# Performance work log

Hardware: AMD Instinct MI355X
Metric: run time of the kernel (lower is better)

Reference implementation:

```python
import jax, jax.numpy as jnp
import numpy as np

D_MODEL = 1024
NUM_HEADS = 16
D_K = D_MODEL // NUM_HEADS
ROPE_THETA = 10000.0


def apply_rope(x, positions):
    # x: (b, h, s, d_k), positions: (b, s) int
    half = D_K // 2
    inv_freq = ROPE_THETA ** (-jnp.arange(half, dtype=jnp.float32) * 2.0 / D_K)  # (half,)
    angles = positions[:, None, :, None].astype(jnp.float32) * inv_freq  # (b,1,s,half)
    cos, sin = jnp.cos(angles), jnp.sin(angles)
    x_even = x[..., 0::2]
    x_odd = x[..., 1::2]
    r_even = x_even * cos - x_odd * sin
    r_odd = x_even * sin + x_odd * cos
    # re-interleave
    out = jnp.stack([r_even, r_odd], axis=-1).reshape(x.shape)
    return out


def setup_inputs() -> dict:
    key = jax.random.key(0)
    k1, k2, k3, k4, k5 = jax.random.split(key, 5)
    b, s = 2, 2048
    scale = 1.0 / np.sqrt(D_MODEL)
    x = jax.random.normal(k1, (b, s, D_MODEL), dtype=jnp.float32)
    w_q = jax.random.normal(k2, (D_MODEL, D_MODEL), dtype=jnp.float32) * scale
    w_k = jax.random.normal(k3, (D_MODEL, D_MODEL), dtype=jnp.float32) * scale
    w_v = jax.random.normal(k4, (D_MODEL, D_MODEL), dtype=jnp.float32) * scale
    w_o = jax.random.normal(k5, (D_MODEL, D_MODEL), dtype=jnp.float32) * scale
    token_positions = jnp.broadcast_to(jnp.arange(s, dtype=jnp.int64 if jax.config.jax_enable_x64 else jnp.int32), (b, s))
    return {"x": x, "w_q": w_q, "w_k": w_k, "w_v": w_v, "w_o": w_o,
            "token_positions": token_positions}


def reference(x, w_q, w_k, w_v, w_o, token_positions):
    b, s, _ = x.shape
    # QKV projections: w_* are (h*d_k, d_model); y = x @ w^T
    def proj(w):
        y = jnp.einsum('bsd,ed->bse', x, w)  # (b,s,h*d_k)
        return y.reshape(b, s, NUM_HEADS, D_K).transpose(0, 2, 1, 3)  # (b,h,s,d_k)
    Q, K, V = proj(w_q), proj(w_k), proj(w_v)
    Q = apply_rope(Q, token_positions)
    K = apply_rope(K, token_positions)
    scores = jnp.einsum('bhqd,bhkd->bhqk', Q, K) / jnp.sqrt(jnp.float32(D_K))
    causal = jnp.tril(jnp.ones((s, s), dtype=bool))
    scores = jnp.where(causal[None, None], scores, -jnp.inf)
    attn = jax.nn.softmax(scores, axis=-1)
    out = jnp.einsum('bhqk,bhkd->bhqd', attn, V)  # (b,h,s,d_v)
    out = out.transpose(0, 2, 1, 3).reshape(b, s, NUM_HEADS * D_K)
    return jnp.einsum('bse,de->bsd', out, w_o)
```

## Files before the change

### kernel.cpp

```cpp
#include <hip/hip_runtime.h>

#define B_ 2
#define S_ 2048
#define DM 1024
#define NH 16
#define DK 64

using bf16x8  = __attribute__((ext_vector_type(8)))  short;
using f32x4   = __attribute__((ext_vector_type(4)))  float;

__device__ __forceinline__ float bf2f(short v){
  unsigned u = ((unsigned)(unsigned short)v) << 16;
  union { unsigned u; float f; } c; c.u = u; return c.f;
}
__device__ __forceinline__ short f2bf(float f){
  union { float f; unsigned u; } c; c.f = f;
  unsigned u = c.u + 0x7FFFu + ((c.u >> 16) & 1u);
  return (short)(u >> 16);
}
__device__ __forceinline__ unsigned packbf(float lo, float hi){
  union { float f; unsigned u; } a, b; a.f = lo; b.f = hi;
  return __builtin_amdgcn_perm(b.u, a.u, 0x07060302u);
}
__device__ __forceinline__ void gload16(const void* g, void* l){
  __builtin_amdgcn_global_load_lds(
    (const __attribute__((address_space(1))) unsigned*)g,
    (__attribute__((address_space(3))) unsigned*)l, 16, 0, 0);
}

__global__ void cast_rope(const float* __restrict__ x, const float* __restrict__ wq,
                          const float* __restrict__ wk, const float* __restrict__ wv,
                          const float* __restrict__ wo, const int* __restrict__ pos,
                          short* __restrict__ xb, short* __restrict__ wqkv,
                          short* __restrict__ wob, float* __restrict__ tab){
  const int bid = blockIdx.x;
  if (bid < 8192){
    int i = bid * 256 + threadIdx.x;
    const float4* src; short4* dst;
    if (i < (1 << 20)){
      src = (const float4*)x + i; dst = (short4*)xb + i;
    } else {
      int j = i - (1 << 20);
      int seg = j >> 18, off = j & ((1 << 18) - 1);
      const float* sp = seg == 0 ? wq : seg == 1 ? wk : seg == 2 ? wv : wo;
      short* dp = seg < 3 ? wqkv + ((size_t)seg << 20) : wob;
      src = (const float4*)sp + off; dst = (short4*)dp + off;
    }
    float4 v = *src;
    short4 o; o.x = f2bf(v.x); o.y = f2bf(v.y); o.z = f2bf(v.z); o.w = f2bf(v.w);
    *dst = o;
  } else {
    int idx = (bid - 8192) * 256 + threadIdx.x;
    int j = idx & 31, bs = idx >> 5;
    float p = (float)pos[bs];
    float inv = powf(10000.0f, -(float)(2 * j) / 64.0f);
    float ang = p * inv;
    tab[(size_t)bs * 64 + j]      = cosf(ang);
    tab[(size_t)bs * 64 + 32 + j] = sinf(ang);
  }
}

__launch_bounds__(512)
__global__ void gemm_qkv(const short* __restrict__ A, const short* __restrict__ Bm,
                         const float* __restrict__ tab,
                         short* __restrict__ Qr, short* __restrict__ Kr,
                         short* __restrict__ Vt){
  __shared__ short lds[3 * 8192];
  constexpr int K = 1024, NT = 32;
  const int tid = threadIdx.x;
  const int l = tid & 63, w = tid >> 6;
  const int lr = l & 15, lg = l >> 4;
  const int wr = w >> 2, wc = w & 3;
  const int wg  = blockIdx.y * gridDim.x + blockIdx.x;
  const int xcd = wg & 7, idx = wg >> 3;
  const int bn  = (xcd & 1) * 12 + idx % 12;
  const int bm  = (xcd >> 1) * 8 + idx / 12;
  const short* Ab = A  + (size_t)bm * 128 * K;
  const short* Bb = Bm + (size_t)bn * 128 * K;
  const int r0 = tid >> 2, c4 = tid & 3;
  f32x4 acc[4][2];
  #pragma unroll
  for (int m = 0; m < 4; ++m)
    #pragma unroll
    for (int n = 0; n < 2; ++n) acc[m][n] = (f32x4){0.f, 0.f, 0.f, 0.f};

  auto stage = [&](int t){
    short* buf = lds + (t % 3) * 8192;
    gload16(Ab + (size_t)r0 * K + t * 32 + c4 * 8, buf + tid * 8);
    gload16(Bb + (size_t)r0 * K + t * 32 + c4 * 8, buf + 4096 + tid * 8);
  };

  stage(0); stage(1);
  for (int t = 0; t < NT; ++t){
    if (t < NT - 1) asm volatile("s_waitcnt vmcnt(2)" ::: "memory");
    else            asm volatile("s_waitcnt vmcnt(0)" ::: "memory");
    __builtin_amdgcn_s_barrier();
    __builtin_amdgcn_sched_barrier(0);
    if (t + 2 < NT) stage(t + 2);
    const short* bufA = lds + (t % 3) * 8192;
    const short* bufB = bufA + 4096;
    bf16x8 a[4], bfr[2];
    #pragma unroll
    for (int m = 0; m < 4; ++m)
      a[m] = *(const bf16x8*)(bufA + (wr * 64 + m * 16 + lr) * 32 + lg * 8);
    #pragma unroll
    for (int n = 0; n < 2; ++n)
      bfr[n] = *(const bf16x8*)(bufB + (wc * 32 + n * 16 + lr) * 32 + lg * 8);
    __builtin_amdgcn_s_setprio(1);
    #pragma unroll
    for (int m = 0; m < 4; ++m)
      #pragma unroll
      for (int n = 0; n < 2; ++n)
        acc[m][n] = __builtin_amdgcn_mfma_f32_16x16x32_bf16(a[m], bfr[n], acc[m][n], 0, 0, 0);
    __builtin_amdgcn_s_setprio(0);
  }

  if (bn >= 16){
    __syncthreads();
    short* T = lds;
    #pragma unroll
    for (int m = 0; m < 4; ++m)
      #pragma unroll
      for (int n = 0; n < 2; ++n){
        const int col_l = wc * 32 + n * 16 + lr;
        const int row0  = wr * 64 + m * 16 + lg * 4;
        short4 pk;
        pk.x = f2bf(acc[m][n][0]); pk.y = f2bf(acc[m][n][1]);
        pk.z = f2bf(acc[m][n][2]); pk.w = f2bf(acc[m][n][3]);
        *(short4*)(T + col_l * 136 + row0) = pk;
      }
    __syncthreads();
    const int h0   = (bn - 16) * 2;
    const int tok0 = bm * 128;
    const int b    = tok0 >> 11, s0 = tok0 & 2047;
    const int col_l = tid >> 2;
    const int d  = col_l & 63;
    const int hh = h0 + (col_l >> 6);
    short* dstrow = Vt + ((size_t)(b * NH + hh) * DK + d) * S_ + s0;
    #pragma unroll
    for (int k = 0; k < 4; ++k){
      const int chunk = (tid & 3) * 4 + k;
      bf16x8 v = *(const bf16x8*)(T + col_l * 136 + chunk * 8);
      *(bf16x8*)(dstrow + chunk * 8) = v;
    }
  } else {
    #pragma unroll
    for (int m = 0; m < 4; ++m)
      #pragma unroll
      for (int n = 0; n < 2; ++n){
        const int col = bn * 128 + wc * 32 + n * 16 + lr;
        const int which = col >> 10;
        #pragma unroll
        for (int j = 0; j < 4; ++j){
          const int row = bm * 128 + wr * 64 + m * 16 + lg * 4 + j;
          float v = acc[m][n][j];
          const int d  = col & 63;
          const int dp = d >> 1;
          const float c = tab[(size_t)row * 64 + dp];
          const float s = tab[(size_t)row * 64 + 32 + dp];
          const float p = __shfl_xor(v, 1);
          float r = v * c + p * ((d & 1) ? s : -s);
          if (which == 0) r *= 0.125f;
          short* dst = which ? Kr : Qr;
          const int b = row >> 11, si = row & 2047;
          const int h = (col >> 6) & 15;
          dst[(((size_t)(b * NH + h)) * S_ + si) * DK + d] = f2bf(r);
        }
      }
  }
}

__launch_bounds__(512)
__global__ void gemm_o(const short* __restrict__ A, const short* __restrict__ Bm,
                       float* __restrict__ C){
  __shared__ short As[128 * 32];
  __shared__ short Bs[64 * 32];
  constexpr int K = 1024, N = 1024;
  const int tid = threadIdx.x;
  const int l = tid & 63, w = tid >> 6;
  const int lr = l & 15, lg = l >> 4;
  const int wr = w >> 2, wc = w & 3;
  const int nwg = gridDim.x * gridDim.y;
  const int wg  = blockIdx.y * gridDim.x + blockIdx.x;
  const int sw  = (wg & 7) * (nwg >> 3) + (wg >> 3);
  const int bn  = sw % gridDim.x, bm = sw / gridDim.x;
  const short* Ab = A  + (size_t)bm * 128 * K;
  const short* Bb = Bm + (size_t)bn * 64 * K;
  f32x4 acc[4];
  #pragma unroll
  for (int m = 0; m < 4; ++m) acc[m] = (f32x4){0.f, 0.f, 0.f, 0.f};
  const int r0 = tid >> 2, c4 = tid & 3;
  for (int kt = 0; kt < K; kt += 32){
    gload16(Ab + (size_t)r0 * K + kt + c4 * 8, As + tid * 8);
    if (tid < 256)
      gload16(Bb + (size_t)r0 * K + kt + c4 * 8, Bs + tid * 8);
    __syncthreads();
    bf16x8 a[4], bfr;
    #pragma unroll
    for (int m = 0; m < 4; ++m)
      a[m] = *(const bf16x8*)(As + (wr * 64 + m * 16 + lr) * 32 + lg * 8);
    bfr = *(const bf16x8*)(Bs + (wc * 16 + lr) * 32 + lg * 8);
    #pragma unroll
    for (int m = 0; m < 4; ++m)
      acc[m] = __builtin_amdgcn_mfma_f32_16x16x32_bf16(a[m], bfr, acc[m], 0, 0, 0);
    __syncthreads();
  }
  #pragma unroll
  for (int m = 0; m < 4; ++m)
    #pragma unroll
    for (int j = 0; j < 4; ++j){
      int row = bm * 128 + wr * 64 + m * 16 + lg * 4 + j;
      int col = bn * 64 + wc * 16 + lr;
      C[(size_t)row * N + col] = acc[m][j];
    }
}

__device__ __forceinline__ void attn_tile_step(
    const bf16x8 qa0, const bf16x8 qa1,
    f32x4 (&acc)[4], float& mrow, float& lsum,
    const short* Ks, const short* Vs, unsigned* pw,
    int diagmask, int lr, int lg, int wl){
  float sv[4][4];
  __builtin_amdgcn_s_setprio(1);
  #pragma unroll
  for (int n = 0; n < 4; ++n){
    const int R = n * 16 + lr;
    const int c0 = lg ^ (R & 7);
    bf16x8 k0 = *(const bf16x8*)(Ks + R * 64 + c0 * 8);
    bf16x8 k1 = *(const bf16x8*)(Ks + R * 64 + (c0 ^ 4) * 8);
    f32x4 z = (f32x4){0.f, 0.f, 0.f, 0.f};
    z = __builtin_amdgcn_mfma_f32_16x16x32_bf16(k0, qa0, z, 0, 0, 0);
    z = __builtin_amdgcn_mfma_f32_16x16x32_bf16(k1, qa1, z, 0, 0, 0);
    #pragma unroll
    for (int j = 0; j < 4; ++j) sv[n][j] = z[j];
  }
  __builtin_amdgcn_s_setprio(0);
  if (diagmask){
    const int qloc = wl * 16 + lr;
    #pragma unroll
    for (int n = 0; n < 4; ++n)
      #pragma unroll
      for (int j = 0; j < 4; ++j)
        if (n * 16 + lg * 4 + j > qloc) sv[n][j] = -1e30f;
  }
  float lm = sv[0][0];
  #pragma unroll
  for (int n = 0; n < 4; ++n)
    #pragma unroll
    for (int j = 0; j < 4; ++j) lm = fmaxf(lm, sv[n][j]);
  lm = fmaxf(lm, __shfl_xor(lm, 16));
  lm = fmaxf(lm, __shfl_xor(lm, 32));
  if (!__all(lm <= mrow + 8.f)){
    float mnew = fmaxf(mrow, lm);
    float corr = __expf(mrow - mnew);
    mrow = mnew;
    lsum *= corr;
    float cb[4];
    #pragma unroll
    for (int j = 0; j < 4; ++j) cb[j] = __shfl(corr, lg * 4 + j);
    #pragma unroll
    for (int n = 0; n < 4; ++n)
      #pragma unroll
      for (int j = 0; j < 4; ++j) acc[n][j] *= cb[j];
  }
  float psum = 0.f;
  #pragma unroll
  for (int n = 0; n < 4; ++n)
    #pragma unroll
    for (int j = 0; j < 4; ++j){
      float p = __expf(sv[n][j] - mrow);
      sv[n][j] = p; psum += p;
    }
  psum += __shfl_xor(psum, 16);
  psum += __shfl_xor(psum, 32);
  lsum += psum;
  const int swz = (lr & 7) << 2;
  #pragma unroll
  for (int n = 0; n < 4; ++n){
    pw[lr * 32 + ((n * 8 + lg * 2 + 0) ^ swz)] = packbf(sv[n][0], sv[n][1]);
    pw[lr * 32 + ((n * 8 + lg * 2 + 1) ^ swz)] = packbf(sv[n][2], sv[n][3]);
  }
  bf16x8 pa0 = *(const bf16x8*)(pw + lr * 32 + ((lg * 4) ^ swz));
  bf16x8 pa1 = *(const bf16x8*)(pw + lr * 32 + ((16 + lg * 4) ^ swz));
  __builtin_amdgcn_s_setprio(1);
  #pragma unroll
  for (int n = 0; n < 4; ++n){
    const int R = n * 16 + lr;
    const int c0 = lg ^ (R & 7);
    bf16x8 v0 = *(const bf16x8*)(Vs + R * 64 + c0 * 8);
    bf16x8 v1 = *(const bf16x8*)(Vs + R * 64 + (c0 ^ 4) * 8);
    acc[n] = __builtin_amdgcn_mfma_f32_16x16x32_bf16(pa0, v0, acc[n], 0, 0, 0);
    acc[n] = __builtin_amdgcn_mfma_f32_16x16x32_bf16(pa1, v1, acc[n], 0, 0, 0);
  }
  __builtin_amdgcn_s_setprio(0);
}

__launch_bounds__(512)
__global__ void attn_kernel(const short* __restrict__ Qr, const short* __restrict__ Kr,
                            const short* __restrict__ Vt, short* __restrict__ AO){
  __shared__ short Ks[2][64 * 64];
  __shared__ short Vs[2][64 * 64];
  __shared__ unsigned Pw[8][16 * 32];
  const int tid = threadIdx.x;
  const int l = tid & 63, w = tid >> 6;
  const int lr = l & 15, lg = l >> 4;
  const int wl = w & 3, wgp = w >> 2;
  const int bid = blockIdx.x;
  const int qp = bid >> 5;
  const int bh = (((bid >> 3) & 3) << 3) | (bid & 7);
  const int h = bh & 15, b = bh >> 4;
  const int t0 = qp, t1 = 31 - qp;
  const int myqt = wgp ? t0 : t1;
  const short* Qp = Qr + (size_t)bh * S_ * DK;
  const short* Kp = Kr + (size_t)bh * S_ * DK;
  const short* Vp = Vt + (size_t)bh * DK * S_;

  bf16x8 qa0, qa1;
  {
    const short* q0 = Qp + (size_t)(myqt * 64 + wl * 16 + lr) * DK + lg * 8;
    qa0 = *(const bf16x8*)q0; qa1 = *(const bf16x8*)(q0 + 32);
  }
  f32x4 acc[4];
  float ms = -1e30f, ls = 0.f;
  #pragma unroll
  for (int n = 0; n < 4; ++n) acc[n] = (f32x4){0.f, 0.f, 0.f, 0.f};
  unsigned* pw = &Pw[w][0];
  const int r0 = tid >> 3, q8 = tid & 7;
  const int sq8 = q8 ^ (r0 & 7);

  gload16(Kp + (size_t)r0 * DK + sq8 * 8, &Ks[0][tid * 8]);
  gload16(Vp + (size_t)r0 * S_ + sq8 * 8, &Vs[0][tid * 8]);
  int cur = 0;
  for (int kt = 0; kt <= t1; ++kt){
    __syncthreads();
    if (kt < t1){
      gload16(Kp + (size_t)((kt + 1) * 64 + r0) * DK + sq8 * 8, &Ks[cur ^ 1][tid * 8]);
      gload16(Vp + (size_t)r0 * S_ + (kt + 1) * 64 + sq8 * 8,   &Vs[cur ^ 1][tid * 8]);
    }
    if (kt <= myqt)
      attn_tile_step(qa0, qa1, acc, ms, ls, Ks[cur], Vs[cur], pw, kt == myqt, lr, lg, wl);
    cur ^= 1;
  }
  const float li = 1.f / ls;
  #pragma unroll
  for (int j = 0; j < 4; ++j){
    const float d0 = __shfl(li, lg * 4 + j);
    #pragma unroll
    for (int n = 0; n < 4; ++n){
      int e = h * 64 + n * 16 + lr;
      int r = myqt * 64 + wl * 16 + lg * 4 + j;
      AO[((size_t)b * S_ + r) * DM + e] = f2bf(acc[n][j] * d0);
    }
  }
}

extern "C" void kernel_launch(void* const* d_in, const int* in_sizes, int n_in,
                              void* d_out, int out_size, void* d_ws, size_t ws_size,
                              hipStream_t stream){
  const float* x  = (const float*)d_in[0];
  const float* wq = (const float*)d_in[1];
  const float* wk = (const float*)d_in[2];
  const float* wv = (const float*)d_in[3];
  const float* wo = (const float*)d_in[4];
  const int*  pos = (const int*)d_in[5];

  char* ws = (char*)d_ws;
  short* xb   = (short*)(ws + 0);
  short* wqkv = (short*)(ws + ((size_t)8  << 20));
  short* wob  = (short*)(ws + ((size_t)14 << 20));
  short* Qr   = (short*)(ws + ((size_t)40 << 20));
  short* Kr   = (short*)(ws + ((size_t)48 << 20));
  short* Vt   = (short*)(ws + ((size_t)56 << 20));
  float* tab  = (float*)(ws + ((size_t)64 << 20));
  short* AO   = xb;
  float* out  = (float*)d_out;

  cast_rope<<<dim3(8704), dim3(256), 0, stream>>>(x, wq, wk, wv, wo, pos, xb, wqkv, wob, tab);
  gemm_qkv<<<dim3(24, 32), dim3(512), 0, stream>>>(xb, wqkv, tab, Qr, Kr, Vt);
  attn_kernel<<<dim3(512), dim3(512), 0, stream>>>(Qr, Kr, Vt, AO);
  gemm_o<<<dim3(16, 32), dim3(512), 0, stream>>>(AO, wob, out);
}
```

Measured before the change: 114.9 us.

## Triple-buffer output projection GEMM loads and drop setprio in attention

The output-projection GEMM moves from a single LDS buffer with two barriers per k-step to a three-stage ring buffer. Direct-to-LDS global loads are issued two tiles ahead, with vmcnt waits and one barrier per step, so load latency overlaps MFMA work. The MFMA section of the GEMM gets raised wave priority, while the setprio calls are removed from the attention tile step. The ring buffer uses more LDS, and the hand-placed waitcnts assume an exact count of outstanding loads per thread.

```diff
diff --git a/kernel.cpp b/kernel.cpp
--- a/kernel.cpp
+++ b/kernel.cpp
@@ -173,9 +173,8 @@
 __launch_bounds__(512)
 __global__ void gemm_o(const short* __restrict__ A, const short* __restrict__ Bm,
                        float* __restrict__ C){
-  __shared__ short As[128 * 32];
-  __shared__ short Bs[64 * 32];
-  constexpr int K = 1024, N = 1024;
+  __shared__ short lds[3 * 6144];
+  constexpr int K = 1024, N = 1024, NT = 32;
   const int tid = threadIdx.x;
   const int l = tid & 63, w = tid >> 6;
   const int lr = l & 15, lg = l >> 4;
@@ -186,24 +185,39 @@
   const int bn  = sw % gridDim.x, bm = sw / gridDim.x;
   const short* Ab = A  + (size_t)bm * 128 * K;
   const short* Bb = Bm + (size_t)bn * 64 * K;
+  const int r0 = tid >> 2, c4 = tid & 3;
   f32x4 acc[4];
   #pragma unroll
   for (int m = 0; m < 4; ++m) acc[m] = (f32x4){0.f, 0.f, 0.f, 0.f};
-  const int r0 = tid >> 2, c4 = tid & 3;
-  for (int kt = 0; kt < K; kt += 32){
-    gload16(Ab + (size_t)r0 * K + kt + c4 * 8, As + tid * 8);
+
+  auto stage = [&](int t){
+    short* buf = lds + (t % 3) * 6144;
+    gload16(Ab + (size_t)r0 * K + t * 32 + c4 * 8, buf + tid * 8);
     if (tid < 256)
-      gload16(Bb + (size_t)r0 * K + kt + c4 * 8, Bs + tid * 8);
-    __syncthreads();
+      gload16(Bb + (size_t)r0 * K + t * 32 + c4 * 8, buf + 4096 + tid * 8);
+  };
+
+  stage(0); stage(1);
+  for (int t = 0; t < NT; ++t){
+    if (t < NT - 1){
+      if (tid < 256) asm volatile("s_waitcnt vmcnt(2)" ::: "memory");
+      else           asm volatile("s_waitcnt vmcnt(1)" ::: "memory");
+    } else           asm volatile("s_waitcnt vmcnt(0)" ::: "memory");
+    __builtin_amdgcn_s_barrier();
+    __builtin_amdgcn_sched_barrier(0);
+    if (t + 2 < NT) stage(t + 2);
+    const short* bufA = lds + (t % 3) * 6144;
+    const short* bufB = bufA + 4096;
     bf16x8 a[4], bfr;
     #pragma unroll
     for (int m = 0; m < 4; ++m)
-      a[m] = *(const bf16x8*)(As + (wr * 64 + m * 16 + lr) * 32 + lg * 8);
-    bfr = *(const bf16x8*)(Bs + (wc * 16 + lr) * 32 + lg * 8);
+      a[m] = *(const bf16x8*)(bufA + (wr * 64 + m * 16 + lr) * 32 + lg * 8);
+    bfr = *(const bf16x8*)(bufB + (wc * 16 + lr) * 32 + lg * 8);
+    __builtin_amdgcn_s_setprio(1);
     #pragma unroll
     for (int m = 0; m < 4; ++m)
       acc[m] = __builtin_amdgcn_mfma_f32_16x16x32_bf16(a[m], bfr, acc[m], 0, 0, 0);
-    __syncthreads();
+    __builtin_amdgcn_s_setprio(0);
   }
   #pragma unroll
   for (int m = 0; m < 4; ++m)
@@ -221,7 +235,6 @@
     const short* Ks, const short* Vs, unsigned* pw,
     int diagmask, int lr, int lg, int wl){
   float sv[4][4];
-  __builtin_amdgcn_s_setprio(1);
   #pragma unroll
   for (int n = 0; n < 4; ++n){
     const int R = n * 16 + lr;
@@ -234,7 +247,6 @@
     #pragma unroll
     for (int j = 0; j < 4; ++j) sv[n][j] = z[j];
   }
-  __builtin_amdgcn_s_setprio(0);
   if (diagmask){
     const int qloc = wl * 16 + lr;
     #pragma unroll
@@ -282,7 +294,6 @@
   }
   bf16x8 pa0 = *(const bf16x8*)(pw + lr * 32 + ((lg * 4) ^ swz));
   bf16x8 pa1 = *(const bf16x8*)(pw + lr * 32 + ((16 + lg * 4) ^ swz));
-  __builtin_amdgcn_s_setprio(1);
   #pragma unroll
   for (int n = 0; n < 4; ++n){
     const int R = n * 16 + lr;
@@ -292,7 +303,6 @@
     acc[n] = __builtin_amdgcn_mfma_f32_16x16x32_bf16(pa0, v0, acc[n], 0, 0, 0);
     acc[n] = __builtin_amdgcn_mfma_f32_16x16x32_bf16(pa1, v1, acc[n], 0, 0, 0);
   }
-  __builtin_amdgcn_s_setprio(0);
 }
 
 __launch_bounds__(512)
```

After: 111.0 us, median of 2. 1.04x faster.
